# Kernel optimization log

Hardware: AMD Instinct MI355X
Metric: run time of the kernel (lower is better)

## Reference

```python
import jax, jax.numpy as jnp
import numpy as np

B, P, D = 8, 576, 1024
H = 16
HD = D // H  # 64
HID = 4 * D  # 4096
EPS = 1e-6  # flax LayerNorm default


def _ln(x, g, b):
    m = jnp.mean(x, axis=-1, keepdims=True)
    v = jnp.var(x, axis=-1, keepdims=True)
    return (x - m) * jax.lax.rsqrt(v + EPS) * g + b


def setup_inputs() -> dict:
    key = jax.random.key(0)
    ks = jax.random.split(key, 8)
    s = 0.02
    return {
        "x": jax.random.normal(ks[0], (B, P, D), dtype=jnp.float32),
        "w_qkv": jax.random.normal(ks[1], (D, 3 * D), dtype=jnp.float32) * s,
        "q_g": jnp.ones((HD,), jnp.float32), "q_b": jnp.zeros((HD,), jnp.float32),
        "k_g": jnp.ones((HD,), jnp.float32), "k_b": jnp.zeros((HD,), jnp.float32),
        "o_g": jnp.ones((D,), jnp.float32), "o_b": jnp.zeros((D,), jnp.float32),
        "w_proj": jax.random.normal(ks[2], (D, D), dtype=jnp.float32) * s,
        "b_proj": jnp.zeros((D,), jnp.float32),
        "ln1_g": jnp.ones((D,), jnp.float32), "ln1_b": jnp.zeros((D,), jnp.float32),
        "ln2_g": jnp.ones((D,), jnp.float32), "ln2_b": jnp.zeros((D,), jnp.float32),
        "w1": jax.random.normal(ks[3], (D, HID), dtype=jnp.float32) * s,
        "b1": jnp.zeros((HID,), jnp.float32),
        "w2": jax.random.normal(ks[4], (HID, D), dtype=jnp.float32) * s,
        "b2": jnp.zeros((D,), jnp.float32),
        "ls1": jnp.full((D,), 1e-5, jnp.float32),
        "ls2": jnp.full((D,), 1e-5, jnp.float32),
    }


def reference(x, w_qkv, q_g, q_b, k_g, k_b, o_g, o_b, w_proj, b_proj,
              ln1_g, ln1_b, ln2_g, ln2_b, w1, b1, w2, b2, ls1, ls2):
    scale = HD ** (-0.5)
    # --- attention branch ---
    o = _ln(x, ln1_g, ln1_b)
    qkv = jnp.einsum('bpd,de->bpe', o, w_qkv)
    qkv = qkv.reshape(B, P, 3, H, HD).transpose(2, 0, 3, 1, 4)  # [3,B,H,P,HD]
    q, k, v = qkv[0], qkv[1], qkv[2]
    q = _ln(q, q_g, q_b) * scale  # QK-LayerNorm per head
    k = _ln(k, k_g, k_b)
    attn = jax.nn.softmax(jnp.einsum('bhqd,bhkd->bhqk', q, k), axis=-1)
    o = jnp.einsum('bhqk,bhkd->bhqd', attn, v)
    o = jnp.swapaxes(o, 1, 2).reshape(B, P, D)
    o = _ln(o, o_g, o_b)
    o = jnp.einsum('bpd,de->bpe', o, w_proj) + b_proj
    x = x + o * ls1
    # --- MLP branch ---
    o = _ln(x, ln2_g, ln2_b)
    o = jax.nn.gelu(jnp.einsum('bpd,dh->bph', o, w1) + b1)  # tanh-approx gelu (flax default)
    o = jnp.einsum('bph,hd->bpd', o, w2) + b2
    return x + o * ls2
```

## Files before the change

kernel.cpp:

```cpp
#include <hip/hip_runtime.h>
#include <hip/hip_bf16.h>

#define DEV static __device__ __forceinline__

typedef short frag8 __attribute__((ext_vector_type(8)));
typedef float accf4 __attribute__((ext_vector_type(4)));


DEV unsigned short f2bf(float f){
  union { float f; unsigned int u; } v; v.f = f;
  unsigned int r = v.u + 0x7fffu + ((v.u >> 16) & 1u);
  return (unsigned short)(r >> 16);
}

DEV float bf2f(unsigned short u){
  union { unsigned int i; float f; } v; v.i = (unsigned int)u << 16; return v.f;
}

DEV void gload16(const void* g, void* l){
  __builtin_amdgcn_global_load_lds((const __attribute__((address_space(1))) void*)g,
                                   (__attribute__((address_space(3))) void*)l, 16, 0, 0);
}

DEV float gelu_tanh(float x){
  float u = 0.7978845608028654f * (x + 0.044715f * x * x * x);
  float e = __expf(2.0f * u);
  float th = 1.0f - 2.0f / (e + 1.0f);
  return 0.5f * x * (1.0f + th);
}

DEV void block_map(int bid, int nwg, int gx, int& tx, int& ty){
  const int swz = ((nwg & 7) == 0) ? ((bid & 7) * (nwg >> 3) + (bid >> 3)) : bid;
  const int gy = nwg / gx;
  const int cg = swz / (gy * 16);
  const int rr = swz - cg * gy * 16;
  const int gw = min(16, gx - cg * 16);
  tx = cg * 16 + rr % gw;
  ty = rr / gw;
}

__global__ __launch_bounds__(256) void wtrans_all(
    const float* __restrict__ Wq, unsigned short* __restrict__ Tq,
    const float* __restrict__ Wp, unsigned short* __restrict__ Tp,
    const float* __restrict__ W1, unsigned short* __restrict__ T1,
    const float* __restrict__ W2, unsigned short* __restrict__ T2){
  __shared__ float t[32][33];
  const int id = blockIdx.x;
  const float* W; unsigned short* Wt; int K, N, idx;
  if (id < 3072)      { W = Wq; Wt = Tq; K = 1024; N = 3072; idx = id; }
  else if (id < 4096) { W = Wp; Wt = Tp; K = 1024; N = 1024; idx = id - 3072; }
  else if (id < 8192) { W = W1; Wt = T1; K = 1024; N = 4096; idx = id - 4096; }
  else                { W = W2; Wt = T2; K = 4096; N = 1024; idx = id - 8192; }
  const int ntx = N >> 5;
  const int n0 = (idx % ntx) * 32, k0 = (idx / ntx) * 32;
  const int tx = threadIdx.x, ty = threadIdx.y;
  #pragma unroll
  for (int i = 0; i < 4; i++)
    t[ty + i*8][tx] = W[(long)(k0 + ty + i*8) * N + n0 + tx];
  __syncthreads();
  #pragma unroll
  for (int i = 0; i < 4; i++)
    Wt[(long)(n0 + ty + i*8) * K + k0 + tx] = f2bf(t[tx][ty + i*8]);
}

template<int BF>
__global__ __launch_bounds__(256) void ln_rows(const void* __restrict__ inp,
                                               const float* __restrict__ g,
                                               const float* __restrict__ beta,
                                               unsigned short* __restrict__ out){
  const long row = blockIdx.x;
  const int t = threadIdx.x;
  float4 v;
  if constexpr (BF){
    const ushort4 u = ((const ushort4*)inp)[row * 256 + t];
    v.x = bf2f(u.x); v.y = bf2f(u.y); v.z = bf2f(u.z); v.w = bf2f(u.w);
  } else {
    v = ((const float4*)inp)[row * 256 + t];
  }
  float s  = v.x + v.y + v.z + v.w;
  float s2 = v.x*v.x + v.y*v.y + v.z*v.z + v.w*v.w;
  #pragma unroll
  for (int o = 32; o; o >>= 1){ s += __shfl_xor(s, o); s2 += __shfl_xor(s2, o); }
  __shared__ float rs[4], rq[4];
  const int wv = t >> 6;
  if ((t & 63) == 0){ rs[wv] = s; rq[wv] = s2; }
  __syncthreads();
  s  = rs[0] + rs[1] + rs[2] + rs[3];
  s2 = rq[0] + rq[1] + rq[2] + rq[3];
  const float mean = s * (1.f/1024.f);
  const float inv = rsqrtf(s2 * (1.f/1024.f) - mean*mean + 1e-6f);
  const float4 gv = ((const float4*)g)[t];
  const float4 bv = ((const float4*)beta)[t];
  ushort4 o4;
  o4.x = f2bf((v.x - mean)*inv*gv.x + bv.x);
  o4.y = f2bf((v.y - mean)*inv*gv.y + bv.y);
  o4.z = f2bf((v.z - mean)*inv*gv.z + bv.z);
  o4.w = f2bf((v.w - mean)*inv*gv.w + bv.w);
  *(ushort4*)(out + row * 1024 + t * 4) = o4;
}

__global__ __launch_bounds__(256) void attn_k(const unsigned short* __restrict__ Qn,
                                              const unsigned short* __restrict__ Kn,
                                              const unsigned short* __restrict__ Vt,
                                              unsigned short* __restrict__ O){
  __shared__ __align__(16) unsigned short Ks[2][4096];
  __shared__ __align__(16) unsigned short Vs[2][4096];
  __shared__ __align__(16) unsigned short Plds[4096];
  const int f = blockIdx.x;
  const int xcd = f & 7, j = f >> 3;
  const int bh = xcd * 16 + j / 9;
  const int qb = j - (j / 9) * 9;
  const int b = bh >> 4, h = bh & 15;
  const int tid = threadIdx.x, w = tid >> 6, l = tid & 63;
  const int fr = l & 15, fq = l >> 4;
  const int rsw = fr & 7;
  const int q0 = qb * 64;

  const unsigned short* qbase = Qn + ((long)bh * 576 + q0 + w * 16 + fr) * 64;
  const frag8 qf0 = *(const frag8*)(qbase + fq * 8);
  const frag8 qf1 = *(const frag8*)(qbase + 32 + fq * 8);

  const int r8 = l >> 3;
  const int kq8 = ((l & 7) ^ r8) * 8;
  const unsigned short* kSrc = Kn + ((long)bh * 576 + w * 16 + r8) * 64 + kq8;
  const unsigned short* vSrc = Vt + ((long)bh * 64 + w * 16 + r8) * 576 + kq8;

  auto stage = [&](int d, int t){
    gload16(kSrc + (long)t * 4096,              &Ks[d][w * 1024]);
    gload16(kSrc + (long)t * 4096 + 512,        &Ks[d][w * 1024 + 512]);
    gload16(vSrc + (long)t * 64,                &Vs[d][w * 1024]);
    gload16(vSrc + (long)t * 64 + 8l * 576,     &Vs[d][w * 1024 + 512]);
  };

  accf4 oacc[4];
  #pragma unroll
  for (int nd = 0; nd < 4; nd++) oacc[nd] = (accf4){0.f, 0.f, 0.f, 0.f};
  float m[4] = {-1e30f, -1e30f, -1e30f, -1e30f};
  float lsum[4] = {0.f, 0.f, 0.f, 0.f};

  stage(0, 0);
  __syncthreads();
  int cur = 0;
  for (int t = 0; t < 9; ++t){
    if (t < 8) stage(cur ^ 1, t + 1);

    accf4 st[4];
    #pragma unroll
    for (int kt4 = 0; kt4 < 4; kt4++){
      const int c0 = ((0 * 4 + fq) ^ rsw) * 8;
      const int c1 = ((1 * 4 + fq) ^ rsw) * 8;
      frag8 kf0 = *(const frag8*)&Ks[cur][(kt4 * 16 + fr) * 64 + c0];
      frag8 kf1 = *(const frag8*)&Ks[cur][(kt4 * 16 + fr) * 64 + c1];
      accf4 a = {0.f, 0.f, 0.f, 0.f};
      a = __builtin_amdgcn_mfma_f32_16x16x32_bf16(qf0, kf0, a, 0, 0, 0);
      a = __builtin_amdgcn_mfma_f32_16x16x32_bf16(qf1, kf1, a, 0, 0, 0);
      st[kt4] = a;
    }

    #pragma unroll
    for (int rr = 0; rr < 4; rr++){
      float v = fmaxf(fmaxf(st[0][rr], st[1][rr]), fmaxf(st[2][rr], st[3][rr]));
      #pragma unroll
      for (int o = 8; o; o >>= 1) v = fmaxf(v, __shfl_xor(v, o));
      const float mn = fmaxf(m[rr], v);
      const float sc = __expf(m[rr] - mn);
      float p[4], rs = 0.f;
      #pragma unroll
      for (int kt4 = 0; kt4 < 4; kt4++){ p[kt4] = __expf(st[kt4][rr] - mn); rs += p[kt4]; }
      #pragma unroll
      for (int o = 8; o; o >>= 1) rs += __shfl_xor(rs, o);
      lsum[rr] = lsum[rr] * sc + rs;
      m[rr] = mn;
      #pragma unroll
      for (int nd = 0; nd < 4; nd++) oacc[nd][rr] *= sc;
      const int prow = fq * 4 + rr;
      #pragma unroll
      for (int kt4 = 0; kt4 < 4; kt4++){
        const int chunk = kt4 * 2 + (fr >> 3);
        Plds[w * 1024 + prow * 64 + ((chunk ^ (prow & 7)) << 3) + (fr & 7)] = f2bf(p[kt4]);
      }
    }

    #pragma unroll
    for (int nd = 0; nd < 4; nd++){
      const int c0 = ((0 * 4 + fq) ^ rsw) * 8;
      const int c1 = ((1 * 4 + fq) ^ rsw) * 8;
      frag8 af0 = *(const frag8*)&Plds[w * 1024 + fr * 64 + c0];
      frag8 af1 = *(const frag8*)&Plds[w * 1024 + fr * 64 + c1];
      frag8 vf0 = *(const frag8*)&Vs[cur][(nd * 16 + fr) * 64 + c0];
      frag8 vf1 = *(const frag8*)&Vs[cur][(nd * 16 + fr) * 64 + c1];
      oacc[nd] = __builtin_amdgcn_mfma_f32_16x16x32_bf16(af0, vf0, oacc[nd], 0, 0, 0);
      oacc[nd] = __builtin_amdgcn_mfma_f32_16x16x32_bf16(af1, vf1, oacc[nd], 0, 0, 0);
    }

    __syncthreads();
    cur ^= 1;
  }

  #pragma unroll
  for (int rr = 0; rr < 4; rr++){
    const float rinv = 1.f / lsum[rr];
    const long orow = (long)b * 576 + q0 + w * 16 + fq * 4 + rr;
    #pragma unroll
    for (int nd = 0; nd < 4; nd++)
      O[orow * 1024 + h * 64 + nd * 16 + fr] = f2bf(oacc[nd][rr] * rinv);
  }
}

template<int BN, int EPI>
__global__ __launch_bounds__(256) void gemm_bk64(
    const unsigned short* __restrict__ A, const unsigned short* __restrict__ Bt,
    float* __restrict__ Cf, unsigned short* __restrict__ Cb,
    const float* __restrict__ bias, const float* __restrict__ ls,
    const float* __restrict__ resid,
    const float* __restrict__ qg, const float* __restrict__ qb2,
    const float* __restrict__ kg, const float* __restrict__ kb2,
    unsigned short* __restrict__ Qn, unsigned short* __restrict__ Kn,
    unsigned short* __restrict__ Vt,
    int M, int N, int K, int gx)
{
  constexpr int NF = BN / 32;
  constexpr int BSLOT = BN / 32;
  __shared__ __align__(16) unsigned short As[2][128 * 64];
  __shared__ __align__(16) unsigned short Bs[2][BN * 64];
  const int tid = threadIdx.x;
  const int wave = tid >> 6, l = tid & 63;
  const int fr = l & 15, fq = l >> 4;
  const int wr = wave >> 1, wc = wave & 1;
  const int rsw = fr & 7;
  int tx, ty;
  block_map(blockIdx.x, gridDim.x, gx, tx, ty);
  const long rowbase = (long)ty * 128;
  const long colbase = (long)tx * BN;

  const int r8 = l >> 3;
  const int kq = (l & 7) ^ r8;
  const unsigned short* aS = A + (rowbase + wave*32 + r8) * (long)K + kq * 8;
  const unsigned short* bS = Bt + (colbase + wave*(BN/4) + r8) * (long)K + kq * 8;

  accf4 acc[4][NF];
  const accf4 zero = {0.f, 0.f, 0.f, 0.f};
  #pragma unroll
  for (int m = 0; m < 4; m++)
    #pragma unroll
    for (int n = 0; n < NF; n++) acc[m][n] = zero;

  auto stage = [&](int d, int t){
    const long k0 = (long)t * 64;
    #pragma unroll
    for (int s = 0; s < 4; s++)
      gload16(aS + (long)s * 8 * K + k0, &As[d][(wave*4 + s) * 512]);
    #pragma unroll
    for (int s = 0; s < BSLOT; s++)
      gload16(bS + (long)s * 8 * K + k0, &Bs[d][(wave*BSLOT + s) * 512]);
  };
  auto compute = [&](int d){
    #pragma unroll
    for (int kk = 0; kk < 2; kk++){
      const int csw = ((kk * 4 + fq) ^ rsw) * 8;
      frag8 bf[NF];
      #pragma unroll
      for (int n = 0; n < NF; n++)
        bf[n] = *(const frag8*)&Bs[d][(wc*(BN/2) + n*16 + fr) * 64 + csw];
      #pragma unroll
      for (int m = 0; m < 4; m++){
        frag8 af = *(const frag8*)&As[d][(wr*64 + m*16 + fr) * 64 + csw];
        #pragma unroll
        for (int n = 0; n < NF; n++)
          acc[m][n] = __builtin_amdgcn_mfma_f32_16x16x32_bf16(af, bf[n], acc[m][n], 0, 0, 0);
      }
    }
  };

  const int NT = K >> 6;
  stage(0, 0);
  __syncthreads();
  int cur = 0;
  for (int t = 0; t < NT; ++t){
    if (t + 1 < NT) stage(cur ^ 1, t + 1);
    compute(cur);
    __syncthreads();
    cur ^= 1;
  }

  if constexpr (EPI == 3){
    const int cg = (int)colbase + wc * 64;
    const int kind = cg >> 10;
    const int h = (cg & 1023) >> 6;
    if (kind < 2){
      const float* g  = kind ? kg : qg;
      const float* bb = kind ? kb2 : qb2;
      const float sc = kind ? 1.0f : 0.125f;
      unsigned short* Out = kind ? Kn : Qn;
      #pragma unroll
      for (int m = 0; m < 4; m++){
        #pragma unroll
        for (int r = 0; r < 4; r++){
          float s1 = 0.f, s2 = 0.f;
          #pragma unroll
          for (int n = 0; n < NF; n++){ const float v = acc[m][n][r]; s1 += v; s2 += v*v; }
          #pragma unroll
          for (int o = 8; o; o >>= 1){ s1 += __shfl_xor(s1, o); s2 += __shfl_xor(s2, o); }
          const float mean = s1 * (1.f/64.f);
          const float inv = rsqrtf(s2 * (1.f/64.f) - mean*mean + 1e-6f);
          const long row = rowbase + wr*64 + m*16 + fq*4 + r;
          const int bq = (int)(row / 576), p = (int)(row - (long)bq*576);
          unsigned short* dst = Out + (((long)(bq*16 + h))*576 + p)*64;
          #pragma unroll
          for (int n = 0; n < NF; n++){
            const int d = n*16 + fr;
            dst[d] = f2bf(((acc[m][n][r] - mean)*inv*g[d] + bb[d]) * sc);
          }
        }
      }
    } else {
      #pragma unroll
      for (int m = 0; m < 4; m++){
        const long grow = rowbase + wr*64 + m*16 + fq*4;
        const int bq = (int)(grow / 576), p = (int)(grow - (long)bq*576);
        #pragma unroll
        for (int n = 0; n < NF; n++){
          const int d = n*16 + fr;
          ushort4 o4;
          o4.x = f2bf(acc[m][n][0]); o4.y = f2bf(acc[m][n][1]);
          o4.z = f2bf(acc[m][n][2]); o4.w = f2bf(acc[m][n][3]);
          *(ushort4*)(Vt + ((long)(bq*16 + h)*64 + d)*576 + p) = o4;
        }
      }
    }
  } else {
    #pragma unroll
    for (int m = 0; m < 4; m++){
      const long rb = rowbase + wr * 64 + m * 16 + fq * 4;
      #pragma unroll
      for (int n = 0; n < NF; n++){
        const long cb = colbase + wc * (BN/2) + n * 16 + fr;
        #pragma unroll
        for (int r = 0; r < 4; r++){
          const long idx = (rb + r) * N + cb;
          const float v = acc[m][n][r];
          if constexpr (EPI == 1){
            Cf[idx] = resid[idx] + (v + bias[cb]) * ls[cb];
          } else {
            Cb[idx] = f2bf(gelu_tanh(v + bias[cb]));
          }
        }
      }
    }
  }
}

extern "C" void kernel_launch(void* const* d_in, const int* in_sizes, int n_in,
                              void* d_out, int out_size, void* d_ws, size_t ws_size,
                              hipStream_t stream){
  (void)in_sizes; (void)n_in; (void)out_size; (void)ws_size;
  const float* x      = (const float*)d_in[0];
  const float* w_qkv  = (const float*)d_in[1];
  const float* q_g    = (const float*)d_in[2];
  const float* q_b    = (const float*)d_in[3];
  const float* k_g    = (const float*)d_in[4];
  const float* k_b    = (const float*)d_in[5];
  const float* o_g    = (const float*)d_in[6];
  const float* o_b    = (const float*)d_in[7];
  const float* w_proj = (const float*)d_in[8];
  const float* b_proj = (const float*)d_in[9];
  const float* ln1_g  = (const float*)d_in[10];
  const float* ln1_b  = (const float*)d_in[11];
  const float* ln2_g  = (const float*)d_in[12];
  const float* ln2_b  = (const float*)d_in[13];
  const float* w1     = (const float*)d_in[14];
  const float* b1     = (const float*)d_in[15];
  const float* w2     = (const float*)d_in[16];
  const float* b2     = (const float*)d_in[17];
  const float* ls1    = (const float*)d_in[18];
  const float* ls2    = (const float*)d_in[19];
  float* out = (float*)d_out;

  char* ws = (char*)d_ws;
  size_t off = 0;
  auto alloc = [&](size_t bytes)->void*{
    void* p = ws + off; off += (bytes + 255) & ~(size_t)255; return p;
  };
  unsigned short* wqkvT  = (unsigned short*)alloc(3072l*1024*2);
  unsigned short* wprojT = (unsigned short*)alloc(1024l*1024*2);
  unsigned short* w1T    = (unsigned short*)alloc(4096l*1024*2);
  unsigned short* w2T    = (unsigned short*)alloc(1024l*4096*2);
  unsigned short* xnA    = (unsigned short*)alloc(4608l*1024*2);
  unsigned short* Qn     = (unsigned short*)alloc(73728l*64*2);
  unsigned short* Kn     = (unsigned short*)alloc(73728l*64*2);
  unsigned short* Vt     = (unsigned short*)alloc(73728l*64*2);
  unsigned short* hbf    = (unsigned short*)alloc(4608l*4096*2);
  unsigned short* attnO  = (unsigned short*)alloc(4608l*1024*2);

  wtrans_all<<<12288, dim3(32,8), 0, stream>>>(w_qkv, wqkvT, w_proj, wprojT,
                                               w1, w1T, w2, w2T);

  ln_rows<0><<<4608, 256, 0, stream>>>(x, ln1_g, ln1_b, xnA);
  gemm_bk64<128,3><<<24*36, 256, 0, stream>>>(xnA, wqkvT, nullptr, nullptr,
                                              nullptr, nullptr, nullptr,
                                              q_g, q_b, k_g, k_b, Qn, Kn, Vt,
                                              4608, 3072, 1024, 24);
  attn_k<<<1152, 256, 0, stream>>>(Qn, Kn, Vt, attnO);
  ln_rows<1><<<4608, 256, 0, stream>>>(attnO, o_g, o_b, xnA);
  gemm_bk64<64,1><<<16*36, 256, 0, stream>>>(xnA, wprojT, out, nullptr,
                                             b_proj, ls1, x,
                                             nullptr, nullptr, nullptr, nullptr,
                                             nullptr, nullptr, nullptr,
                                             4608, 1024, 1024, 16);
  ln_rows<0><<<4608, 256, 0, stream>>>(out, ln2_g, ln2_b, xnA);
  gemm_bk64<64,2><<<64*36, 256, 0, stream>>>(xnA, w1T, nullptr, hbf,
                                             b1, nullptr, nullptr,
                                             nullptr, nullptr, nullptr, nullptr,
                                             nullptr, nullptr, nullptr,
                                             4608, 4096, 1024, 64);
  gemm_bk64<64,1><<<16*36, 256, 0, stream>>>(hbf, w2T, out, nullptr,
                                             b2, ls2, out,
                                             nullptr, nullptr, nullptr, nullptr,
                                             nullptr, nullptr, nullptr,
                                             4608, 1024, 4096, 16);
}
```

Measured before the change: 257.9 us.

## Split QK-LayerNorm out of QKV GEMM epilogue and fold LN1 into weight transpose

The QKV GEMM drops from a 128-wide tile with a fused per-head LayerNorm epilogue to a 64-wide tile. That GEMM now writes raw bf16 Q/K to an intermediate buffer, and a new qkln kernel applies the per-head LayerNorm, scaling and head-major relayout. The first row LayerNorm is merged into the weight-transpose launch as extra blocks, removing one kernel launch. The intent is a lighter GEMM epilogue with better occupancy and more blocks. In exchange it adds an extra round trip of the Q/K activations through global memory and one more launch.

New measurement: 275.8 us. +7.0%, slower.

```diff
diff --git a/kernel.cpp b/kernel.cpp
--- a/kernel.cpp
+++ b/kernel.cpp
@@ -43,9 +43,37 @@
     const float* __restrict__ Wq, unsigned short* __restrict__ Tq,
     const float* __restrict__ Wp, unsigned short* __restrict__ Tp,
     const float* __restrict__ W1, unsigned short* __restrict__ T1,
-    const float* __restrict__ W2, unsigned short* __restrict__ T2){
+    const float* __restrict__ W2, unsigned short* __restrict__ T2,
+    const float* __restrict__ x, const float* __restrict__ g1,
+    const float* __restrict__ b1g, unsigned short* __restrict__ xnA){
   __shared__ float t[32][33];
+  __shared__ float rs[4], rq[4];
   const int id = blockIdx.x;
+  if (id >= 12288){
+    const long row = id - 12288;
+    const int tt = threadIdx.y * 32 + threadIdx.x;
+    const float4 v = ((const float4*)x)[row * 256 + tt];
+    float s  = v.x + v.y + v.z + v.w;
+    float s2 = v.x*v.x + v.y*v.y + v.z*v.z + v.w*v.w;
+    #pragma unroll
+    for (int o = 32; o; o >>= 1){ s += __shfl_xor(s, o); s2 += __shfl_xor(s2, o); }
+    const int wv = tt >> 6;
+    if ((tt & 63) == 0){ rs[wv] = s; rq[wv] = s2; }
+    __syncthreads();
+    s  = rs[0] + rs[1] + rs[2] + rs[3];
+    s2 = rq[0] + rq[1] + rq[2] + rq[3];
+    const float mean = s * (1.f/1024.f);
+    const float inv = rsqrtf(s2 * (1.f/1024.f) - mean*mean + 1e-6f);
+    const float4 gv = ((const float4*)g1)[tt];
+    const float4 bv = ((const float4*)b1g)[tt];
+    ushort4 o4;
+    o4.x = f2bf((v.x - mean)*inv*gv.x + bv.x);
+    o4.y = f2bf((v.y - mean)*inv*gv.y + bv.y);
+    o4.z = f2bf((v.z - mean)*inv*gv.z + bv.z);
+    o4.w = f2bf((v.w - mean)*inv*gv.w + bv.w);
+    *(ushort4*)(xnA + row * 1024 + tt * 4) = o4;
+    return;
+  }
   const float* W; unsigned short* Wt; int K, N, idx;
   if (id < 3072)      { W = Wq; Wt = Tq; K = 1024; N = 3072; idx = id; }
   else if (id < 4096) { W = Wp; Wt = Tp; K = 1024; N = 1024; idx = id - 3072; }
@@ -61,6 +89,32 @@
   #pragma unroll
   for (int i = 0; i < 4; i++)
     Wt[(long)(n0 + ty + i*8) * K + k0 + tx] = f2bf(t[tx][ty + i*8]);
+}
+
+__global__ __launch_bounds__(256) void qkln(const unsigned short* __restrict__ qk,
+    const float* __restrict__ qg, const float* __restrict__ qb2,
+    const float* __restrict__ kg, const float* __restrict__ kb2,
+    unsigned short* __restrict__ Qn, unsigned short* __restrict__ Kn){
+  const int lane = threadIdx.x;
+  const int r = blockIdx.x * 4 + threadIdx.y;
+  const int bh = r / 576, p = r - bh * 576;
+  const int b = bh >> 4, h = bh & 15;
+  const long base = ((long)(b * 576 + p)) * 2048 + h * 64 + lane;
+  const float q = bf2f(qk[base]);
+  const float k = bf2f(qk[base + 1024]);
+  float sq = q, sq2 = q*q, sk = k, sk2 = k*k;
+  #pragma unroll
+  for (int o = 32; o; o >>= 1){
+    sq += __shfl_xor(sq, o); sq2 += __shfl_xor(sq2, o);
+    sk += __shfl_xor(sk, o); sk2 += __shfl_xor(sk2, o);
+  }
+  const float mq = sq * (1.f/64.f), vq = sq2 * (1.f/64.f) - mq*mq;
+  const float mk = sk * (1.f/64.f), vk = sk2 * (1.f/64.f) - mk*mk;
+  const float qn = ((q - mq) * rsqrtf(vq + 1e-6f) * qg[lane] + qb2[lane]) * 0.125f;
+  const float kn =  (k - mk) * rsqrtf(vk + 1e-6f) * kg[lane] + kb2[lane];
+  const long ob = (long)r * 64 + lane;
+  Qn[ob] = f2bf(qn);
+  Kn[ob] = f2bf(kn);
 }
 
 template<int BF>
@@ -213,9 +267,6 @@
     float* __restrict__ Cf, unsigned short* __restrict__ Cb,
     const float* __restrict__ bias, const float* __restrict__ ls,
     const float* __restrict__ resid,
-    const float* __restrict__ qg, const float* __restrict__ qb2,
-    const float* __restrict__ kg, const float* __restrict__ kb2,
-    unsigned short* __restrict__ Qn, unsigned short* __restrict__ Kn,
     unsigned short* __restrict__ Vt,
     int M, int N, int K, int gx)
 {
@@ -283,44 +334,29 @@
     cur ^= 1;
   }
 
-  if constexpr (EPI == 3){
-    const int cg = (int)colbase + wc * 64;
-    const int kind = cg >> 10;
-    const int h = (cg & 1023) >> 6;
+  if constexpr (EPI == 5){
+    const int kind = (int)colbase >> 10;
     if (kind < 2){
-      const float* g  = kind ? kg : qg;
-      const float* bb = kind ? kb2 : qb2;
-      const float sc = kind ? 1.0f : 0.125f;
-      unsigned short* Out = kind ? Kn : Qn;
       #pragma unroll
       for (int m = 0; m < 4; m++){
+        const long rb = rowbase + wr * 64 + m * 16 + fq * 4;
         #pragma unroll
-        for (int r = 0; r < 4; r++){
-          float s1 = 0.f, s2 = 0.f;
+        for (int n = 0; n < NF; n++){
+          const long cb = colbase + wc * (BN/2) + n * 16 + fr;
           #pragma unroll
-          for (int n = 0; n < NF; n++){ const float v = acc[m][n][r]; s1 += v; s2 += v*v; }
-          #pragma unroll
-          for (int o = 8; o; o >>= 1){ s1 += __shfl_xor(s1, o); s2 += __shfl_xor(s2, o); }
-          const float mean = s1 * (1.f/64.f);
-          const float inv = rsqrtf(s2 * (1.f/64.f) - mean*mean + 1e-6f);
-          const long row = rowbase + wr*64 + m*16 + fq*4 + r;
-          const int bq = (int)(row / 576), p = (int)(row - (long)bq*576);
-          unsigned short* dst = Out + (((long)(bq*16 + h))*576 + p)*64;
-          #pragma unroll
-          for (int n = 0; n < NF; n++){
-            const int d = n*16 + fr;
-            dst[d] = f2bf(((acc[m][n][r] - mean)*inv*g[d] + bb[d]) * sc);
-          }
+          for (int r = 0; r < 4; r++)
+            Cb[(rb + r) * 2048 + cb] = f2bf(acc[m][n][r]);
         }
       }
     } else {
+      const int h = ((int)colbase - 2048) >> 6;
       #pragma unroll
       for (int m = 0; m < 4; m++){
         const long grow = rowbase + wr*64 + m*16 + fq*4;
         const int bq = (int)(grow / 576), p = (int)(grow - (long)bq*576);
         #pragma unroll
         for (int n = 0; n < NF; n++){
-          const int d = n*16 + fr;
+          const int d = wc*(BN/2) + n*16 + fr;
           ushort4 o4;
           o4.x = f2bf(acc[m][n][0]); o4.y = f2bf(acc[m][n][1]);
           o4.z = f2bf(acc[m][n][2]); o4.w = f2bf(acc[m][n][3]);
@@ -386,36 +422,31 @@
   unsigned short* w1T    = (unsigned short*)alloc(4096l*1024*2);
   unsigned short* w2T    = (unsigned short*)alloc(1024l*4096*2);
   unsigned short* xnA    = (unsigned short*)alloc(4608l*1024*2);
+  unsigned short* QKraw  = (unsigned short*)alloc(4608l*2048*2);
   unsigned short* Qn     = (unsigned short*)alloc(73728l*64*2);
   unsigned short* Kn     = (unsigned short*)alloc(73728l*64*2);
   unsigned short* Vt     = (unsigned short*)alloc(73728l*64*2);
   unsigned short* hbf    = (unsigned short*)alloc(4608l*4096*2);
   unsigned short* attnO  = (unsigned short*)alloc(4608l*1024*2);
 
-  wtrans_all<<<12288, dim3(32,8), 0, stream>>>(w_qkv, wqkvT, w_proj, wprojT,
-                                               w1, w1T, w2, w2T);
-
-  ln_rows<0><<<4608, 256, 0, stream>>>(x, ln1_g, ln1_b, xnA);
-  gemm_bk64<128,3><<<24*36, 256, 0, stream>>>(xnA, wqkvT, nullptr, nullptr,
-                                              nullptr, nullptr, nullptr,
-                                              q_g, q_b, k_g, k_b, Qn, Kn, Vt,
-                                              4608, 3072, 1024, 24);
+  wtrans_all<<<16896, dim3(32,8), 0, stream>>>(w_qkv, wqkvT, w_proj, wprojT,
+                                               w1, w1T, w2, w2T,
+                                               x, ln1_g, ln1_b, xnA);
+
+  gemm_bk64<64,5><<<48*36, 256, 0, stream>>>(xnA, wqkvT, nullptr, QKraw,
+                                             nullptr, nullptr, nullptr, Vt,
+                                             4608, 3072, 1024, 48);
+  qkln<<<18432, dim3(64,4), 0, stream>>>(QKraw, q_g, q_b, k_g, k_b, Qn, Kn);
   attn_k<<<1152, 256, 0, stream>>>(Qn, Kn, Vt, attnO);
   ln_rows<1><<<4608, 256, 0, stream>>>(attnO, o_g, o_b, xnA);
   gemm_bk64<64,1><<<16*36, 256, 0, stream>>>(xnA, wprojT, out, nullptr,
-                                             b_proj, ls1, x,
-                                             nullptr, nullptr, nullptr, nullptr,
-                                             nullptr, nullptr, nullptr,
+                                             b_proj, ls1, x, nullptr,
                                              4608, 1024, 1024, 16);
   ln_rows<0><<<4608, 256, 0, stream>>>(out, ln2_g, ln2_b, xnA);
   gemm_bk64<64,2><<<64*36, 256, 0, stream>>>(xnA, w1T, nullptr, hbf,
-                                             b1, nullptr, nullptr,
-                                             nullptr, nullptr, nullptr, nullptr,
-                                             nullptr, nullptr, nullptr,
+                                             b1, nullptr, nullptr, nullptr,
                                              4608, 4096, 1024, 64);
   gemm_bk64<64,1><<<16*36, 256, 0, stream>>>(hbf, w2T, out, nullptr,
-                                             b2, ls2, out,
-                                             nullptr, nullptr, nullptr, nullptr,
-                                             nullptr, nullptr, nullptr,
+                                             b2, ls2, out, nullptr,
                                              4608, 1024, 4096, 16);
 }
```
